# Kernel tuning notes

Hardware: AMD Instinct MI355X
Metric: run time of the kernel (lower is better)

The kernel has to match this reference:

```python
import jax, jax.numpy as jnp
import numpy as np

V, E, H, B, S = 50000, 256, 256, 64, 2048


def setup_inputs() -> dict:
    key = jax.random.key(0)
    ks = jax.random.split(key, 13)
    u = lambda k, shape: jax.random.uniform(k, shape, jnp.float32) - 0.5
    return {
        "inp": jax.random.randint(ks[0], (B,), 0, V, dtype=jnp.int64),
        "hidden": jax.random.normal(ks[1], (1, B, H), jnp.float32),
        "encoder_outputs": jax.random.normal(ks[2], (B, S, H), jnp.float32),
        "emb": jax.random.normal(ks[3], (V, E), jnp.float32),          # nn.Embedding weight
        "U": u(ks[4], (H, H)),
        "W": u(ks[5], (H, H)),
        "v": u(ks[6], (H, 1)),
        "W_ih": u(ks[7], (H, E)),   # RNN weight_ih_l0
        "W_hh": u(ks[8], (H, H)),   # RNN weight_hh_l0
        "b_ih": u(ks[9], (H,)),
        "b_hh": u(ks[10], (H,)),
        "W_out": u(ks[11], (V, H)),  # output Linear weight
        "b_out": u(ks[12], (V,)),
    }


def reference(inp, hidden, encoder_outputs, emb, U, W, v,
              W_ih, W_hh, b_ih, b_hh, W_out, b_out):
    # embedding lookup: (B, E)
    x = emb[inp]
    word_embs = x[:, None, :]                         # (B, 1, E)
    # Bahdanau additive attention (get_context)
    summed = jnp.tanh(word_embs @ U + encoder_outputs @ W)   # (B, S, H)
    e_ij = summed @ v                                        # (B, S, 1)
    alpha = jax.nn.softmax(e_ij, axis=1)                     # (B, S, 1)
    context = jnp.sum(alpha * encoder_outputs, axis=1)       # (B, H)
    # single tanh-RNN step; NOTE: original code feeds context as initial hidden,
    # ignoring the `hidden` argument when attention is enabled.
    h_new = jnp.tanh(x @ W_ih.T + b_ih + context @ W_hh.T + b_hh)  # (B, H)
    logits = h_new @ W_out.T + b_out                               # (B, V)
    return logits, h_new[None]                                     # hidden: (1, B, H)
```

## Files before the change

kernel.cpp:

```cpp
#include <hip/hip_runtime.h>
#include <hip/hip_bf16.h>
#include <math.h>

#define V_ 50000
#define E_ 256
#define H_ 256
#define B_ 64
#define S_ 2048
#define NCHK 32

typedef __attribute__((ext_vector_type(4))) float f32x4;
typedef __attribute__((ext_vector_type(16))) float f32x16;
typedef __attribute__((ext_vector_type(8))) __bf16 bf16x8;

static __device__ __forceinline__ f32x4 mfma16(bf16x8 a, bf16x8 b, f32x4 c) {
  return __builtin_amdgcn_mfma_f32_16x16x32_bf16(a, b, c, 0, 0, 0);
}
static __device__ __forceinline__ f32x16 mfma32(bf16x8 a, bf16x8 b, f32x16 c) {
  return __builtin_amdgcn_mfma_f32_32x32x16_bf16(a, b, c, 0, 0, 0);
}
static __device__ __forceinline__ float fast_tanh(float x) {
  const float e2 = __expf(2.0f * x);
  return 1.0f - 2.0f / (e2 + 1.0f);
}
static __device__ __forceinline__ void gll16(const float* g, void* l) {
  __builtin_amdgcn_global_load_lds(
      (const __attribute__((address_space(1))) void*)g,
      (__attribute__((address_space(3))) void*)l, 16, 0, 0);
}

__global__ __launch_bounds__(256) void prep_k(
    const int* __restrict__ inp, const float* __restrict__ emb,
    const float* __restrict__ U, const float* __restrict__ W_ih,
    const float* __restrict__ b_ih, const float* __restrict__ b_hh,
    float* __restrict__ xU, float* __restrict__ xWih) {
  const int b = blockIdx.x, h = threadIdx.x;
  __shared__ float xs[H_];
  xs[h] = emb[(size_t)inp[b] * E_ + h];
  __syncthreads();
  float au = 0.f, aw = 0.f;
  const float* __restrict__ wir = W_ih + (size_t)h * E_;
  for (int k = 0; k < H_; k += 4) {
    const float4 x4 = *reinterpret_cast<const float4*>(&xs[k]);
    const float4 w4 = *reinterpret_cast<const float4*>(wir + k);
    aw = fmaf(x4.x, w4.x, aw); aw = fmaf(x4.y, w4.y, aw);
    aw = fmaf(x4.z, w4.z, aw); aw = fmaf(x4.w, w4.w, aw);
    au = fmaf(x4.x, U[(size_t)(k + 0) * H_ + h], au);
    au = fmaf(x4.y, U[(size_t)(k + 1) * H_ + h], au);
    au = fmaf(x4.z, U[(size_t)(k + 2) * H_ + h], au);
    au = fmaf(x4.w, U[(size_t)(k + 3) * H_ + h], au);
  }
  xU[b * H_ + h] = au;
  xWih[b * H_ + h] = aw + b_ih[h] + b_hh[h];
}

__global__ __launch_bounds__(256) void prep_w(
    const float* __restrict__ W, __bf16* __restrict__ wt2) {
  const int idx = blockIdx.x * 256 + threadIdx.x;
  const int k = idx >> 8, col = idx & 255;
  wt2[((size_t)(k >> 3) * 256 + col) * 8 + (k & 7)] = (__bf16)W[(size_t)k * H_ + col];
}

__global__ __launch_bounds__(256, 3) void attn_fused(
    const float* __restrict__ enc, const __bf16* __restrict__ wt2,
    const float* __restrict__ xU, const float* __restrict__ vv,
    float* __restrict__ ctxp, float* __restrict__ mlout) {
  const int t = threadIdx.x;
  const int w = t >> 6, l = t & 63, l31 = l & 31, h5 = l >> 5;

  __shared__ __align__(16) char Aring[16 * 4096];
  __shared__ float ered[4][64];
  __shared__ float wgt[64];
  __shared__ float mlS[2];

  const int ridx = blockIdx.x;
  const int b = blockIdx.y;
  const int s0 = ridx * 64;

  const int srow = t >> 2;
  const int pch = t & 3;
  const int kch = pch ^ ((srow >> 1) & 3);
  const float* __restrict__ encSrc = enc + ((size_t)b * S_ + s0 + srow) * H_ + kch * 4;

#define STAGE(ks_)                                                 \
  gll16(encSrc + (ks_) * 16, Aring + (ks_) * 4096 + w * 1024);     \
  __builtin_amdgcn_sched_barrier(0);

  STAGE(0); STAGE(1); STAGE(2); STAGE(3); STAGE(4); STAGE(5);
  bf16x8 bh[2][2][2];
#pragma unroll
  for (int hh = 0; hh < 2; ++hh)
#pragma unroll
    for (int cf = 0; cf < 2; ++cf) {
      const int col = w * 64 + cf * 32 + l31;
      const int koct = hh * 2 + h5;
      bh[0][hh][cf] = *reinterpret_cast<const bf16x8*>(
          wt2 + ((size_t)koct * 256 + col) * 8);
    }
  __builtin_amdgcn_sched_barrier(0);

  f32x16 acc[2][2];
#pragma unroll
  for (int rf = 0; rf < 2; ++rf)
#pragma unroll
    for (int cf = 0; cf < 2; ++cf) acc[rf][cf] = (f32x16)(0.f);

  const int sxor = (l31 >> 1) & 3;

#pragma unroll
  for (int it = 0; it < 8; ++it) {
    if (it == 0)      asm volatile("s_waitcnt vmcnt(8)" ::: "memory");
    else if (it == 1) asm volatile("s_waitcnt vmcnt(12)" ::: "memory");
    else if (it <= 5) asm volatile("s_waitcnt vmcnt(16)" ::: "memory");
    else if (it == 6) asm volatile("s_waitcnt vmcnt(14)" ::: "memory");
    else              asm volatile("s_waitcnt vmcnt(12)" ::: "memory");
    __builtin_amdgcn_s_barrier();
    __builtin_amdgcn_sched_barrier(0);
    if (it <= 4) { STAGE(2 * it + 6); STAGE(2 * it + 7); }
    const int pb = it & 1;
    if (it < 7) {
#pragma unroll
      for (int hh = 0; hh < 2; ++hh) {
        const int koct = (2 * (it + 1) + hh) * 2 + h5;
#pragma unroll
        for (int cf = 0; cf < 2; ++cf) {
          const int col = w * 64 + cf * 32 + l31;
          bh[pb ^ 1][hh][cf] = *reinterpret_cast<const bf16x8*>(
              wt2 + ((size_t)koct * 256 + col) * 8);
        }
      }
    }
    __builtin_amdgcn_sched_barrier(0);
#pragma unroll
    for (int hh = 0; hh < 2; ++hh) {
      const int ks = 2 * it + hh;
      bf16x8 ab[2];
#pragma unroll
      for (int rf = 0; rf < 2; ++rf) {
        const char* sb = Aring + ks * 4096 + (rf * 32 + l31) * 64;
        const f32x4 c0 = *reinterpret_cast<const f32x4*>(sb + (((2 * h5 + 0) ^ sxor) << 4));
        const f32x4 c1 = *reinterpret_cast<const f32x4*>(sb + (((2 * h5 + 1) ^ sxor) << 4));
        const float xa[8] = {c0[0], c0[1], c0[2], c0[3], c1[0], c1[1], c1[2], c1[3]};
#pragma unroll
        for (int j = 0; j < 8; ++j) ab[rf][j] = (__bf16)xa[j];
      }
#pragma unroll
      for (int rf = 0; rf < 2; ++rf)
#pragma unroll
        for (int cf = 0; cf < 2; ++cf)
          acc[rf][cf] = mfma32(ab[rf], bh[pb][hh][cf], acc[rf][cf]);
    }
  }
#undef STAGE

  float xu[2], vw[2];
#pragma unroll
  for (int cf = 0; cf < 2; ++cf) {
    const int col = w * 64 + cf * 32 + l31;
    xu[cf] = xU[b * H_ + col];
    vw[cf] = vv[col];
  }
  float rs[2][16];
#pragma unroll
  for (int rf = 0; rf < 2; ++rf)
#pragma unroll
    for (int reg = 0; reg < 16; ++reg) {
      float s = 0.f;
#pragma unroll
      for (int cf = 0; cf < 2; ++cf)
        s += fast_tanh(xu[cf] + acc[rf][cf][reg]) * vw[cf];
      rs[rf][reg] = s;
    }
#pragma unroll
  for (int o = 1; o < 32; o <<= 1)
#pragma unroll
    for (int rf = 0; rf < 2; ++rf)
#pragma unroll
      for (int reg = 0; reg < 16; ++reg)
        rs[rf][reg] += __shfl_xor(rs[rf][reg], o);
  if (l31 == 0) {
#pragma unroll
    for (int rf = 0; rf < 2; ++rf)
#pragma unroll
      for (int reg = 0; reg < 16; ++reg)
        ered[w][rf * 32 + (reg & 3) + 8 * (reg >> 2) + 4 * h5] = rs[rf][reg];
  }
  __syncthreads();

  if (t < 64) {
    const float es = ered[0][t] + ered[1][t] + ered[2][t] + ered[3][t];
    float m = es;
#pragma unroll
    for (int o = 1; o < 64; o <<= 1) m = fmaxf(m, __shfl_xor(m, o));
    const float we = __expf(es - m);
    float ls = we;
#pragma unroll
    for (int o = 1; o < 64; o <<= 1) ls += __shfl_xor(ls, o);
    wgt[t] = we;
    if (t == 0) { mlS[0] = m; mlS[1] = ls; }
  }
  __syncthreads();

  {
    const int h = t;
    const int ks2 = h >> 4, c2 = (h >> 2) & 3, e2 = h & 3;
    const char* base = Aring + ks2 * 4096 + e2 * 4;
    float a = 0.f;
#pragma unroll 8
    for (int s = 0; s < 64; ++s) {
      const int pch2 = c2 ^ ((s >> 1) & 3);
      const float ev = *reinterpret_cast<const float*>(
          base + (s >> 4) * 1024 + (s & 15) * 64 + pch2 * 16);
      a = fmaf(wgt[s], ev, a);
    }
    ctxp[((size_t)ridx * B_ + b) * H_ + h] = a;
  }
  if (t < 2) mlout[(ridx * B_ + b) * 2 + t] = mlS[t];
}

__global__ __launch_bounds__(256) void combine_hnew(
    const float* __restrict__ ctxp, const float* __restrict__ mlout,
    const float* __restrict__ xWih, const float* __restrict__ W_hh,
    float* __restrict__ out_h, __bf16* __restrict__ hn) {
  const int b = blockIdx.x, h = threadIdx.x;
  __shared__ float cs[H_];
  float M = -3.4e38f;
#pragma unroll
  for (int cc = 0; cc < NCHK; ++cc) M = fmaxf(M, mlout[(cc * B_ + b) * 2]);
  float num = 0.f, den = 0.f;
#pragma unroll
  for (int cc = 0; cc < NCHK; ++cc) {
    const float mw = __expf(mlout[(cc * B_ + b) * 2] - M);
    den = fmaf(mw, mlout[(cc * B_ + b) * 2 + 1], den);
    num = fmaf(mw, ctxp[((size_t)cc * B_ + b) * H_ + h], num);
  }
  cs[h] = num / den;
  __syncthreads();
  const float* __restrict__ wr = W_hh + (size_t)h * H_;
  float a = xWih[b * H_ + h];
  for (int k = 0; k < H_; k += 4) {
    const float4 w4 = *reinterpret_cast<const float4*>(wr + k);
    const float4 c4 = *reinterpret_cast<const float4*>(&cs[k]);
    a = fmaf(c4.x, w4.x, a); a = fmaf(c4.y, w4.y, a);
    a = fmaf(c4.z, w4.z, a); a = fmaf(c4.w, w4.w, a);
  }
  const float hv = fast_tanh(a);
  out_h[b * H_ + h] = hv;
  hn[b * H_ + h] = (__bf16)hv;
}

__global__ __launch_bounds__(256) void logits_mfma(
    const float* __restrict__ Wout, const float* __restrict__ bout,
    const __bf16* __restrict__ hn, float* __restrict__ logits) {
  const int v0 = blockIdx.x * 64;
  const int t = threadIdx.x;
  const int wv = t >> 6, l = t & 63, l15 = l & 15, lg = l >> 4;

  __shared__ __bf16 Wsub[8][64][32];

  {
    const int srow = t >> 2, sg = t & 3;
    const int wslot = (sg + (srow >> 1)) & 3;
    const int vc = (v0 + srow) < V_ ? (v0 + srow) : (V_ - 1);
    const float* __restrict__ wr = Wout + (size_t)vc * H_ + sg * 8;
#pragma unroll
    for (int ks = 0; ks < 8; ++ks) {
      const float4 f0 = *reinterpret_cast<const float4*>(wr + ks * 32);
      const float4 f1 = *reinterpret_cast<const float4*>(wr + ks * 32 + 4);
      const float xv[8] = {f0.x, f0.y, f0.z, f0.w, f1.x, f1.y, f1.z, f1.w};
      bf16x8 h8;
#pragma unroll
      for (int j = 0; j < 8; ++j) h8[j] = (__bf16)xv[j];
      *reinterpret_cast<bf16x8*>(&Wsub[ks][srow][wslot * 8]) = h8;
    }
  }
  __syncthreads();

  f32x4 acc[4];
#pragma unroll
  for (int i = 0; i < 4; ++i) acc[i] = (f32x4)(0.f);
  const int colb = wv * 16 + l15;
#pragma unroll
  for (int k = 0; k < 8; ++k) {
    const bf16x8 bfrag = *reinterpret_cast<const bf16x8*>(hn + (size_t)colb * H_ + k * 32 + lg * 8);
    bf16x8 ah[4];
#pragma unroll
    for (int rf = 0; rf < 4; ++rf) {
      const int rr = rf * 16 + l15;
      const int slot = (lg + (rr >> 1)) & 3;
      ah[rf] = *reinterpret_cast<const bf16x8*>(&Wsub[k][rr][slot * 8]);
    }
#pragma unroll
    for (int rf = 0; rf < 4; ++rf)
      acc[rf] = mfma16(ah[rf], bfrag, acc[rf]);
  }
#pragma unroll
  for (int rf = 0; rf < 4; ++rf) {
    const int v = v0 + rf * 16 + lg * 4;
    if (v < V_) {
      const float4 bo = *reinterpret_cast<const float4*>(bout + v);
      float4 o;
      o.x = acc[rf][0] + bo.x; o.y = acc[rf][1] + bo.y;
      o.z = acc[rf][2] + bo.z; o.w = acc[rf][3] + bo.w;
      *reinterpret_cast<float4*>(logits + (size_t)colb * V_ + v) = o;
    }
  }
}

extern "C" void kernel_launch(void* const* d_in, const int* in_sizes, int n_in,
                              void* d_out, int out_size, void* d_ws, size_t ws_size,
                              hipStream_t stream) {
  const int*   inp  = (const int*)  d_in[0];
  const float* enc  = (const float*)d_in[2];
  const float* emb  = (const float*)d_in[3];
  const float* U    = (const float*)d_in[4];
  const float* W    = (const float*)d_in[5];
  const float* v    = (const float*)d_in[6];
  const float* W_ih = (const float*)d_in[7];
  const float* W_hh = (const float*)d_in[8];
  const float* b_ih = (const float*)d_in[9];
  const float* b_hh = (const float*)d_in[10];
  const float* Wout = (const float*)d_in[11];
  const float* bout = (const float*)d_in[12];

  float* logits = (float*)d_out;
  float* out_h  = logits + (size_t)B_ * V_;

  float* ws    = (float*)d_ws;
  __bf16* wt2  = (__bf16*)ws;
  float* xU    = ws + 32768;
  float* xWih  = xU + B_ * H_;
  float* ctxp  = xWih + B_ * H_;
  float* mlout = ctxp + (size_t)NCHK * B_ * H_;
  __bf16* hn   = (__bf16*)(mlout + NCHK * B_ * 2);

  prep_k<<<dim3(B_), dim3(256), 0, stream>>>(inp, emb, U, W_ih, b_ih, b_hh, xU, xWih);
  prep_w<<<dim3(H_ * H_ / 256), dim3(256), 0, stream>>>(W, wt2);
  attn_fused<<<dim3(NCHK, B_), dim3(256), 0, stream>>>(enc, wt2, xU, v, ctxp, mlout);
  combine_hnew<<<dim3(B_), dim3(256), 0, stream>>>(ctxp, mlout, xWih, W_hh, out_h, hn);
  logits_mfma<<<dim3((V_ + 63) / 64), dim3(256), 0, stream>>>(Wout, bout, hn, logits);
}
```

Before: 99.64 us.

## Make attention blocks persistent over four chunks with a continuous 8-slot LDS ring

The attention kernel now launches 512 blocks, and each handles four consecutive 64-row chunks of one batch. An 8-slot LDS ring (half the previous size) is refilled continuously across chunk boundaries, so loads for the next chunk overlap the current chunk's epilogue. The context pass now re-reads the encoder rows from global memory (likely cache hits) instead of LDS, because the ring slots have already been overwritten. The smaller LDS footprint allows more blocks per CU, at the cost of a long hand-tuned vmcnt wait schedule that is easy to get wrong, plus extra global reads.

```diff
diff --git a/kernel.cpp b/kernel.cpp
--- a/kernel.cpp
+++ b/kernel.cpp
@@ -28,6 +28,7 @@
       (const __attribute__((address_space(1))) void*)g,
       (__attribute__((address_space(3))) void*)l, 16, 0, 0);
 }
+#define WAITC(n) asm volatile("s_waitcnt vmcnt(%0)" :: "n"(n) : "memory")
 
 __global__ __launch_bounds__(256) void prep_k(
     const int* __restrict__ inp, const float* __restrict__ emb,
@@ -68,90 +69,14 @@
   const int t = threadIdx.x;
   const int w = t >> 6, l = t & 63, l31 = l & 31, h5 = l >> 5;
 
-  __shared__ __align__(16) char Aring[16 * 4096];
+  __shared__ __align__(16) char Aring[8 * 4096];
   __shared__ float ered[4][64];
   __shared__ float wgt[64];
   __shared__ float mlS[2];
 
-  const int ridx = blockIdx.x;
-  const int b = blockIdx.y;
-  const int s0 = ridx * 64;
-
-  const int srow = t >> 2;
-  const int pch = t & 3;
-  const int kch = pch ^ ((srow >> 1) & 3);
-  const float* __restrict__ encSrc = enc + ((size_t)b * S_ + s0 + srow) * H_ + kch * 4;
-
-#define STAGE(ks_)                                                 \
-  gll16(encSrc + (ks_) * 16, Aring + (ks_) * 4096 + w * 1024);     \
-  __builtin_amdgcn_sched_barrier(0);
-
-  STAGE(0); STAGE(1); STAGE(2); STAGE(3); STAGE(4); STAGE(5);
-  bf16x8 bh[2][2][2];
-#pragma unroll
-  for (int hh = 0; hh < 2; ++hh)
-#pragma unroll
-    for (int cf = 0; cf < 2; ++cf) {
-      const int col = w * 64 + cf * 32 + l31;
-      const int koct = hh * 2 + h5;
-      bh[0][hh][cf] = *reinterpret_cast<const bf16x8*>(
-          wt2 + ((size_t)koct * 256 + col) * 8);
-    }
-  __builtin_amdgcn_sched_barrier(0);
-
-  f32x16 acc[2][2];
-#pragma unroll
-  for (int rf = 0; rf < 2; ++rf)
-#pragma unroll
-    for (int cf = 0; cf < 2; ++cf) acc[rf][cf] = (f32x16)(0.f);
-
-  const int sxor = (l31 >> 1) & 3;
-
-#pragma unroll
-  for (int it = 0; it < 8; ++it) {
-    if (it == 0)      asm volatile("s_waitcnt vmcnt(8)" ::: "memory");
-    else if (it == 1) asm volatile("s_waitcnt vmcnt(12)" ::: "memory");
-    else if (it <= 5) asm volatile("s_waitcnt vmcnt(16)" ::: "memory");
-    else if (it == 6) asm volatile("s_waitcnt vmcnt(14)" ::: "memory");
-    else              asm volatile("s_waitcnt vmcnt(12)" ::: "memory");
-    __builtin_amdgcn_s_barrier();
-    __builtin_amdgcn_sched_barrier(0);
-    if (it <= 4) { STAGE(2 * it + 6); STAGE(2 * it + 7); }
-    const int pb = it & 1;
-    if (it < 7) {
-#pragma unroll
-      for (int hh = 0; hh < 2; ++hh) {
-        const int koct = (2 * (it + 1) + hh) * 2 + h5;
-#pragma unroll
-        for (int cf = 0; cf < 2; ++cf) {
-          const int col = w * 64 + cf * 32 + l31;
-          bh[pb ^ 1][hh][cf] = *reinterpret_cast<const bf16x8*>(
-              wt2 + ((size_t)koct * 256 + col) * 8);
-        }
-      }
-    }
-    __builtin_amdgcn_sched_barrier(0);
-#pragma unroll
-    for (int hh = 0; hh < 2; ++hh) {
-      const int ks = 2 * it + hh;
-      bf16x8 ab[2];
-#pragma unroll
-      for (int rf = 0; rf < 2; ++rf) {
-        const char* sb = Aring + ks * 4096 + (rf * 32 + l31) * 64;
-        const f32x4 c0 = *reinterpret_cast<const f32x4*>(sb + (((2 * h5 + 0) ^ sxor) << 4));
-        const f32x4 c1 = *reinterpret_cast<const f32x4*>(sb + (((2 * h5 + 1) ^ sxor) << 4));
-        const float xa[8] = {c0[0], c0[1], c0[2], c0[3], c1[0], c1[1], c1[2], c1[3]};
-#pragma unroll
-        for (int j = 0; j < 8; ++j) ab[rf][j] = (__bf16)xa[j];
-      }
-#pragma unroll
-      for (int rf = 0; rf < 2; ++rf)
-#pragma unroll
-        for (int cf = 0; cf < 2; ++cf)
-          acc[rf][cf] = mfma32(ab[rf], bh[pb][hh][cf], acc[rf][cf]);
-    }
-  }
-#undef STAGE
+  const int bx = blockIdx.x;
+  const int b = bx >> 3;
+  const int u0 = (bx & 7) * 4;
 
   float xu[2], vw[2];
 #pragma unroll
@@ -160,62 +85,162 @@
     xu[cf] = xU[b * H_ + col];
     vw[cf] = vv[col];
   }
-  float rs[2][16];
-#pragma unroll
-  for (int rf = 0; rf < 2; ++rf)
-#pragma unroll
-    for (int reg = 0; reg < 16; ++reg) {
-      float s = 0.f;
-#pragma unroll
-      for (int cf = 0; cf < 2; ++cf)
-        s += fast_tanh(xu[cf] + acc[rf][cf][reg]) * vw[cf];
-      rs[rf][reg] = s;
-    }
-#pragma unroll
-  for (int o = 1; o < 32; o <<= 1)
+  __builtin_amdgcn_sched_barrier(0);
+  asm volatile("s_waitcnt vmcnt(0)" ::: "memory");
+
+  const int srow = t >> 2;
+  const int pch = t & 3;
+  const int kch = pch ^ ((srow >> 1) & 3);
+  const float* __restrict__ base = enc + ((size_t)b * S_ + srow) * H_ + kch * 4;
+
+#define STAGEG(slot_, addr_)                                    \
+  gll16((addr_), Aring + (slot_) * 4096 + w * 1024);            \
+  __builtin_amdgcn_sched_barrier(0);
+
+#pragma unroll
+  for (int g = 0; g < 6; ++g) {
+    STAGEG(g & 7, base + (size_t)u0 * 16384 + g * 16);
+  }
+  bf16x8 bh[2][2];
+#pragma unroll
+  for (int cf = 0; cf < 2; ++cf) {
+    const int col = w * 64 + cf * 32 + l31;
+    bh[0][cf] = *reinterpret_cast<const bf16x8*>(wt2 + ((size_t)h5 * 256 + col) * 8);
+  }
+  __builtin_amdgcn_sched_barrier(0);
+
+  const int sxor = (l31 >> 1) & 3;
+
+#pragma unroll 1
+  for (int u = 0; u < 4; ++u) {
+    const int ridxu = u0 + u;
+
+    f32x16 acc[2][2];
 #pragma unroll
     for (int rf = 0; rf < 2; ++rf)
 #pragma unroll
-      for (int reg = 0; reg < 16; ++reg)
-        rs[rf][reg] += __shfl_xor(rs[rf][reg], o);
-  if (l31 == 0) {
+      for (int cf = 0; cf < 2; ++cf) acc[rf][cf] = (f32x16)(0.f);
+
+#pragma unroll
+    for (int ks = 0; ks < 16; ++ks) {
+      if (u == 0) {
+        if      (ks == 0) WAITC(7);
+        else if (ks == 1) WAITC(9);
+        else if (ks == 2) WAITC(11);
+        else if (ks == 3) WAITC(13);
+        else if (ks == 4) WAITC(15);
+        else              WAITC(17);
+      } else if (u == 3) {
+        if      (ks == 0) WAITC(0);
+        else if (ks == 1) WAITC(3);
+        else if (ks == 2) WAITC(6);
+        else if (ks == 3) WAITC(9);
+        else if (ks == 4) WAITC(12);
+        else if (ks == 5) WAITC(15);
+        else if (ks <= 10) WAITC(17);
+        else if (ks == 11) WAITC(16);
+        else if (ks == 12) WAITC(15);
+        else if (ks == 13) WAITC(14);
+        else if (ks == 14) WAITC(13);
+        else               WAITC(12);
+      } else {
+        if      (ks == 0) WAITC(0);
+        else if (ks == 1) WAITC(3);
+        else if (ks == 2) WAITC(6);
+        else if (ks == 3) WAITC(9);
+        else if (ks == 4) WAITC(12);
+        else if (ks == 5) WAITC(15);
+        else              WAITC(17);
+      }
+      __builtin_amdgcn_s_barrier();
+      __builtin_amdgcn_sched_barrier(0);
+
+      if (!(u == 3 && ks >= 10)) {
+        const int gslot = (ks + 6) & 7;
+        const int ridx_g = ridxu + ((ks + 6) >> 4);
+        STAGEG(gslot, base + (size_t)ridx_g * 16384 + ((ks + 6) & 15) * 16);
+      }
+      const int pb = ks & 1;
+      if (!(u == 3 && ks == 15)) {
+        const int ks2 = (ks + 1) & 15;
+#pragma unroll
+        for (int cf = 0; cf < 2; ++cf) {
+          const int col = w * 64 + cf * 32 + l31;
+          bh[pb ^ 1][cf] = *reinterpret_cast<const bf16x8*>(
+              wt2 + ((size_t)(2 * ks2 + h5) * 256 + col) * 8);
+        }
+      }
+      __builtin_amdgcn_sched_barrier(0);
+
+      bf16x8 ab[2];
+#pragma unroll
+      for (int rf = 0; rf < 2; ++rf) {
+        const char* sb = Aring + (ks & 7) * 4096 + (rf * 32 + l31) * 64;
+        const f32x4 c0 = *reinterpret_cast<const f32x4*>(sb + (((2 * h5 + 0) ^ sxor) << 4));
+        const f32x4 c1 = *reinterpret_cast<const f32x4*>(sb + (((2 * h5 + 1) ^ sxor) << 4));
+        const float xa[8] = {c0[0], c0[1], c0[2], c0[3], c1[0], c1[1], c1[2], c1[3]};
+#pragma unroll
+        for (int j = 0; j < 8; ++j) ab[rf][j] = (__bf16)xa[j];
+      }
+#pragma unroll
+      for (int rf = 0; rf < 2; ++rf)
+#pragma unroll
+        for (int cf = 0; cf < 2; ++cf)
+          acc[rf][cf] = mfma32(ab[rf], bh[pb][cf], acc[rf][cf]);
+    }
+
+    float rs[2][16];
 #pragma unroll
     for (int rf = 0; rf < 2; ++rf)
 #pragma unroll
-      for (int reg = 0; reg < 16; ++reg)
-        ered[w][rf * 32 + (reg & 3) + 8 * (reg >> 2) + 4 * h5] = rs[rf][reg];
-  }
-  __syncthreads();
-
-  if (t < 64) {
-    const float es = ered[0][t] + ered[1][t] + ered[2][t] + ered[3][t];
-    float m = es;
-#pragma unroll
-    for (int o = 1; o < 64; o <<= 1) m = fmaxf(m, __shfl_xor(m, o));
-    const float we = __expf(es - m);
-    float ls = we;
-#pragma unroll
-    for (int o = 1; o < 64; o <<= 1) ls += __shfl_xor(ls, o);
-    wgt[t] = we;
-    if (t == 0) { mlS[0] = m; mlS[1] = ls; }
-  }
-  __syncthreads();
-
-  {
-    const int h = t;
-    const int ks2 = h >> 4, c2 = (h >> 2) & 3, e2 = h & 3;
-    const char* base = Aring + ks2 * 4096 + e2 * 4;
-    float a = 0.f;
+      for (int reg = 0; reg < 16; ++reg) {
+        float s = 0.f;
+#pragma unroll
+        for (int cf = 0; cf < 2; ++cf)
+          s += fast_tanh(xu[cf] + acc[rf][cf][reg]) * vw[cf];
+        rs[rf][reg] = s;
+      }
+#pragma unroll
+    for (int o = 1; o < 32; o <<= 1)
+#pragma unroll
+      for (int rf = 0; rf < 2; ++rf)
+#pragma unroll
+        for (int reg = 0; reg < 16; ++reg)
+          rs[rf][reg] += __shfl_xor(rs[rf][reg], o);
+    if (l31 == 0) {
+#pragma unroll
+      for (int rf = 0; rf < 2; ++rf)
+#pragma unroll
+        for (int reg = 0; reg < 16; ++reg)
+          ered[w][rf * 32 + (reg & 3) + 8 * (reg >> 2) + 4 * h5] = rs[rf][reg];
+    }
+    __syncthreads();
+
+    if (t < 64) {
+      const float es = ered[0][t] + ered[1][t] + ered[2][t] + ered[3][t];
+      float m = es;
+#pragma unroll
+      for (int o = 1; o < 64; o <<= 1) m = fmaxf(m, __shfl_xor(m, o));
+      const float we = __expf(es - m);
+      float ls = we;
+#pragma unroll
+      for (int o = 1; o < 64; o <<= 1) ls += __shfl_xor(ls, o);
+      wgt[t] = we;
+      if (t == 0) { mlS[0] = m; mlS[1] = ls; }
+    }
+    __syncthreads();
+
+    {
+      const float* __restrict__ ep = enc + ((size_t)b * S_ + ridxu * 64) * H_ + t;
+      float a = 0.f;
 #pragma unroll 8
-    for (int s = 0; s < 64; ++s) {
-      const int pch2 = c2 ^ ((s >> 1) & 3);
-      const float ev = *reinterpret_cast<const float*>(
-          base + (s >> 4) * 1024 + (s & 15) * 64 + pch2 * 16);
-      a = fmaf(wgt[s], ev, a);
-    }
-    ctxp[((size_t)ridx * B_ + b) * H_ + h] = a;
-  }
-  if (t < 2) mlout[(ridx * B_ + b) * 2 + t] = mlS[t];
+      for (int s = 0; s < 64; ++s) a = fmaf(wgt[s], ep[(size_t)s * H_], a);
+      ctxp[((size_t)ridxu * B_ + b) * H_ + t] = a;
+    }
+    if (t < 2) mlout[(ridxu * B_ + b) * 2 + t] = mlS[t];
+    asm volatile("s_waitcnt vmcnt(0)" ::: "memory");
+  }
+#undef STAGEG
 }
 
 __global__ __launch_bounds__(256) void combine_hnew(
@@ -336,7 +361,7 @@
 
   prep_k<<<dim3(B_), dim3(256), 0, stream>>>(inp, emb, U, W_ih, b_ih, b_hh, xU, xWih);
   prep_w<<<dim3(H_ * H_ / 256), dim3(256), 0, stream>>>(W, wt2);
-  attn_fused<<<dim3(NCHK, B_), dim3(256), 0, stream>>>(enc, wt2, xU, v, ctxp, mlout);
+  attn_fused<<<dim3(512), dim3(256), 0, stream>>>(enc, wt2, xU, v, ctxp, mlout);
   combine_hnew<<<dim3(B_), dim3(256), 0, stream>>>(ctxp, mlout, xWih, W_hh, out_h, hn);
   logits_mfma<<<dim3((V_ + 63) / 64), dim3(256), 0, stream>>>(Wout, bout, hn, logits);
 }
```

Measured after the change: 129.1 us. 29.6% more time.
